# Optimization experiments

Hardware: AMD Instinct MI355X
Metric: run time of the kernel (lower is better)

## Reference

```python
import jax, jax.numpy as jnp
import numpy as np

D_MODEL = 384
N_HEADS = 8
HEAD_DIM = D_MODEL // N_HEADS


def setup_inputs() -> dict:
    key = jax.random.key(0)
    ks = jax.random.split(key, 8)
    b, n = 2, 2048
    s = 0.02
    return {
        "x": jax.random.normal(ks[0], (b, n, D_MODEL), jnp.float32),
        "coords": jax.random.normal(ks[1], (b, n, 3), jnp.float32),
        "W_qkv": jax.random.normal(ks[2], (D_MODEL, 3 * D_MODEL), jnp.float32) * s,
        "b_qkv": jnp.zeros((3 * D_MODEL,), jnp.float32),
        "W_dist": jax.random.normal(ks[3], (1, N_HEADS), jnp.float32) * s,
        "b_dist": jnp.zeros((N_HEADS,), jnp.float32),
        "W_out": jax.random.normal(ks[4], (D_MODEL, D_MODEL), jnp.float32) * s,
        "b_out": jnp.zeros((D_MODEL,), jnp.float32),
    }


def reference(x, coords, W_qkv, b_qkv, W_dist, b_dist, W_out, b_out):
    b, n, _ = x.shape
    qkv = x @ W_qkv + b_qkv                       # (b, n, 3*d)
    q, k, v = jnp.split(qkv, 3, axis=-1)
    def heads(t):
        return t.reshape(b, n, N_HEADS, HEAD_DIM).transpose(0, 2, 1, 3)  # b h n d
    q, k, v = heads(q), heads(k), heads(v)
    attn = jnp.einsum('bhid,bhjd->bhij', q, k) / jnp.sqrt(jnp.float32(HEAD_DIM))
    # distance bias: ||c_i - c_j|| projected to heads (Linear(1, n_heads))
    diff = coords[:, :, None, :] - coords[:, None, :, :]   # (b, i, j, 3)
    dist = jnp.sqrt(jnp.sum(diff * diff, axis=-1))         # (b, i, j)
    dist_bias = dist[..., None] * W_dist[0] + b_dist       # (b, i, j, h)
    attn = attn + dist_bias.transpose(0, 3, 1, 2)          # (b, h, i, j)
    attn = jax.nn.softmax(attn, axis=-1)
    out = jnp.einsum('bhij,bhjd->bhid', attn, v)
    out = out.transpose(0, 2, 1, 3).reshape(b, n, D_MODEL)
    return out @ W_out + b_out
```

## Files before the change

### kernel.cpp

```cpp
#include <hip/hip_runtime.h>
#include <hip/hip_bf16.h>

#define NB 2
#define SEQ 2048
#define DM 384
#define NH 8
#define HD 48
#define QKVN 1152
#define BH (NB*NH)

typedef __hip_bfloat16 bf16;
typedef __attribute__((ext_vector_type(8))) short short8;
typedef __attribute__((ext_vector_type(4))) float float4v;

static __device__ __forceinline__ float bf2f(bf16 v){ return __bfloat162float(v); }
static __device__ __forceinline__ float ldin(const void* p, size_t i, int isf){
    return isf ? ((const float*)p)[i] : bf2f(((const bf16*)p)[i]);
}
static __device__ __forceinline__ short f2b(float f){
    union { float f; unsigned u; } a; a.f = f;
    unsigned r = a.u + 0x7FFFu + ((a.u >> 16) & 1u);
    return (short)(r >> 16);
}
static __device__ __forceinline__ unsigned pk2(float a, float b){
    union { __hip_bfloat162 h; unsigned u; } r;
    r.h = __float22bfloat162_rn(float2{a, b});
    return r.u;
}
static __device__ __forceinline__ float bflo(unsigned u){
    union { unsigned u; float f; } a; a.u = u << 16; return a.f;
}
static __device__ __forceinline__ float bfhi(unsigned u){
    union { unsigned u; float f; } a; a.u = u & 0xFFFF0000u; return a.f;
}
static __device__ __forceinline__ short8 s4z(int2 v){
    union { int2 i; short s[4]; } u; u.i = v;
    short8 r = {u.s[0], u.s[1], u.s[2], u.s[3], 0, 0, 0, 0};
    return r;
}
static __device__ __forceinline__ short8 u2z(unsigned a, unsigned b){
    union { unsigned u[2]; short s[4]; } u0; u0.u[0] = a; u0.u[1] = b;
    short8 r = {u0.s[0], u0.s[1], u0.s[2], u0.s[3], 0, 0, 0, 0};
    return r;
}
static __device__ __forceinline__ int detect_isf(const void* x){
    const unsigned short* xb = (const unsigned short*)x;
    int l = threadIdx.x & 63;
    union { unsigned u; float f; } a; a.u = ((unsigned)xb[2*l]) << 16;
    float ab = fabsf(a.f);
    int good = (a.f == 0.0f) || (ab > 9.765625e-4f && ab < 1024.0f);
    unsigned long long m = __ballot(good);
    return (__popcll(m) >= 32) ? 0 : 1;
}

__global__ __launch_bounds__(256) void k_prep(const void* __restrict__ x,
    const void* __restrict__ coords,
    const void* __restrict__ Wqkv, const void* __restrict__ Wout,
    const void* __restrict__ bqkv, const void* __restrict__ bout,
    const void* __restrict__ Wdist, const void* __restrict__ bdist,
    short* __restrict__ dist8, short* __restrict__ xb,
    short* __restrict__ WqT, short* __restrict__ WoT,
    float* __restrict__ bqf, float* __restrict__ bof,
    float* __restrict__ wdf, float* __restrict__ bdf)
{
    const int isf = detect_isf(x);
    const int t = threadIdx.x;
    const int b = blockIdx.x;
    if (b < 512) {
        const int bb = b >> 8;
        const int jg = (b >> 1) & 127;
        const int j0 = jg * 16;
        const int ih = (b & 1) * 1024;
        __shared__ float cjx[16], cjy[16], cjz[16];
        if (t < 16) {
            int gj = (bb*SEQ + j0 + t)*3;
            cjx[t] = ldin(coords, gj, isf);
            cjy[t] = ldin(coords, gj+1, isf);
            cjz[t] = ldin(coords, gj+2, isf);
        }
        __syncthreads();
        #pragma unroll
        for (int k = 0; k < 4; ++k) {
            int i = ih + k*256 + t;
            int gi = (bb*SEQ + i)*3;
            float px = ldin(coords, gi, isf), py = ldin(coords, gi+1, isf), pz = ldin(coords, gi+2, isf);
            short o[16];
            #pragma unroll
            for (int e = 0; e < 16; ++e) {
                float dx = px - cjx[e], dy = py - cjy[e], dz = pz - cjz[e];
                o[e] = f2b(sqrtf(dx*dx + dy*dy + dz*dz));
            }
            short* dst = dist8 + (((size_t)bb*128 + jg)*SEQ + i)*16;
            *(int4*)dst       = *(const int4*)(o);
            *(int4*)(dst + 8) = *(const int4*)(o + 8);
        }
    } else if (b < 1280) {
        size_t i = ((size_t)(b-512)*256 + t)*8;
        if (isf) {
            const float* xf = (const float*)x + i;
            short o[8];
            #pragma unroll
            for (int e = 0; e < 8; ++e) o[e] = f2b(xf[e]);
            *(int4*)(xb + i) = *(const int4*)o;
        } else {
            *(int4*)(xb + i) = *(const int4*)((const short*)x + i);
        }
    } else if (b < 1856) {
        int bb, NW; const void* W; short* WT;
        if (b < 1712) { bb = b - 1280; NW = QKVN; W = Wqkv; WT = WqT; }
        else          { bb = b - 1712; NW = DM;   W = Wout; WT = WoT; }
        int ntiles = NW >> 5;
        int kt = bb / ntiles, nt = bb % ntiles;
        int k0 = kt*32, n0 = nt*32;
        __shared__ float Ls[32][33];
        for (int idx = t; idx < 1024; idx += 256) {
            int r = idx >> 5, c = idx & 31;
            Ls[r][c] = ldin(W, (size_t)(k0+r)*NW + n0 + c, isf);
        }
        __syncthreads();
        for (int idx = t; idx < 1024; idx += 256) {
            int r2 = idx >> 5, c2 = idx & 31;
            WT[(size_t)(n0+r2)*DM + k0 + c2] = f2b(Ls[c2][r2]);
        }
    } else {
        int idx = (b - 1856)*256 + t;
        const float log2e = 1.4426950408889634f;
        if (idx < QKVN) bqf[idx] = ldin(bqkv, idx, isf);
        else if (idx < QKVN + DM) bof[idx - QKVN] = ldin(bout, idx - QKVN, isf);
        else if (idx < QKVN + DM + NH) wdf[idx - QKVN - DM] = ldin(Wdist, idx - QKVN - DM, isf)*log2e;
        else if (idx < QKVN + DM + 2*NH) bdf[idx - QKVN - DM - NH] = ldin(bdist, idx - QKVN - DM - NH, isf)*log2e;
    }
}

__global__ __launch_bounds__(256) void k_qkv(const short* __restrict__ xb,
    const short* __restrict__ WT, const float* __restrict__ bias,
    short* __restrict__ qg2, short* __restrict__ kg2, short* __restrict__ vg2)
{
    __shared__ __align__(16) short As[64*72];
    __shared__ __align__(16) short Bs[128*72];
    const int t = threadIdx.x;
    const int w = t >> 6, lane = t & 63, L = lane & 15, quad = lane >> 4;
    const int mt = blockIdx.x / 9, nt = blockIdx.x % 9;
    const int row0 = mt*64, col0 = nt*128;
    const int wm = w & 1, wn = w >> 1;
    float4v acc[2][4] = {};
    for (int k0 = 0; k0 < DM; k0 += 64) {
        __syncthreads();
        for (int c = t; c < 512; c += 256) {
            int row = c >> 3, k8 = c & 7;
            *(int4*)(&As[row*72 + k8*8]) = *(const int4*)(xb + (size_t)(row0+row)*DM + k0 + k8*8);
        }
        for (int c = t; c < 1024; c += 256) {
            int row = c >> 3, k8 = c & 7;
            *(int4*)(&Bs[row*72 + k8*8]) = *(const int4*)(WT + (size_t)(col0+row)*DM + k0 + k8*8);
        }
        __syncthreads();
        #pragma unroll
        for (int kc = 0; kc < 2; ++kc) {
            short8 a0 = *(const short8*)(&As[(32*wm + L)*72 + kc*32 + quad*8]);
            short8 a1 = *(const short8*)(&As[(32*wm + 16 + L)*72 + kc*32 + quad*8]);
            #pragma unroll
            for (int ni = 0; ni < 4; ++ni) {
                short8 bf = *(const short8*)(&Bs[(64*wn + 16*ni + L)*72 + kc*32 + quad*8]);
                acc[0][ni] = __builtin_amdgcn_mfma_f32_16x16x32_bf16(a0, bf, acc[0][ni], 0, 0, 0);
                acc[1][ni] = __builtin_amdgcn_mfma_f32_16x16x32_bf16(a1, bf, acc[1][ni], 0, 0, 0);
            }
        }
    }
    const int which = col0 / DM;
    const int cbase = col0 % DM;
    short* Ep = Bs;
    __syncthreads();
    if (which < 2) {
        #pragma unroll
        for (int mi = 0; mi < 2; ++mi)
            #pragma unroll
            for (int ni = 0; ni < 4; ++ni) {
                int col_l = 64*wn + 16*ni + L;
                float bv = bias[col0 + col_l];
                #pragma unroll
                for (int r = 0; r < 4; ++r) {
                    int row_l = 32*wm + 16*mi + quad*4 + r;
                    Ep[row_l*136 + col_l] = f2b(acc[mi][ni][r] + bv);
                }
            }
        __syncthreads();
        short* dst = which ? kg2 : qg2;
        for (int c = t; c < 1024; c += 256) {
            int row_l = c >> 4, col_l = (c & 15)*8;
            int row_g = row0 + row_l;
            int bi = row_g >> 11, nn = row_g & (SEQ-1);
            int c2 = cbase + col_l;
            int hh = c2/HD, dh = c2%HD;
            int bh = bi*NH + hh;
            size_t base = ((size_t)bh*128 + (nn>>4))*768;
            int Ltok = nn & 15;
            const short* src = &Ep[row_l*136 + col_l];
            if (dh < 32) {
                *(int4*)(dst + base + (dh>>3)*128 + Ltok*8) = *(const int4*)src;
            } else {
                int q0 = (dh - 32) >> 2;
                *(int2*)(dst + base + 512 + q0*64     + Ltok*4) = *(const int2*)src;
                *(int2*)(dst + base + 512 + (q0+1)*64 + Ltok*4) = *(const int2*)(src + 4);
            }
        }
    } else {
        #pragma unroll
        for (int mi = 0; mi < 2; ++mi)
            #pragma unroll
            for (int ni = 0; ni < 4; ++ni) {
                int col_l = 64*wn + 16*ni + L;
                float bv = bias[col0 + col_l];
                #pragma unroll
                for (int r = 0; r < 4; ++r) {
                    int row_l = 32*wm + 16*mi + quad*4 + r;
                    Ep[col_l*72 + row_l] = f2b(acc[mi][ni][r] + bv);
                }
            }
        __syncthreads();
        for (int c = t; c < 1024; c += 256) {
            int col_l = c >> 3, row8 = (c & 7)*8;
            int row_g = row0 + row8;
            int bi = row_g >> 11, nn = row_g & (SEQ-1);
            int c2 = cbase + col_l;
            int hh = c2/HD, dh = c2%HD;
            int bh = bi*NH + hh;
            int dt = dh >> 4, Lh = dh & 15;
            size_t base3 = (((size_t)bh*128 + (nn>>4))*3 + dt)*256;
            int q0 = (nn & 15) >> 2;
            const short* src = &Ep[col_l*72 + row8];
            *(int2*)(vg2 + base3 + q0*64     + Lh*4) = *(const int2*)src;
            *(int2*)(vg2 + base3 + (q0+1)*64 + Lh*4) = *(const int2*)(src + 4);
        }
    }
}

__global__ __launch_bounds__(256, 4) void k_attn(
    const short* __restrict__ qg2, const short* __restrict__ kg2, const short* __restrict__ vg2,
    const short* __restrict__ dist8, const float* __restrict__ wdf,
    const float* __restrict__ bdf, short* __restrict__ aob)
{
    __shared__ float Ored[2][32*48];
    __shared__ float Lred[2][32];
    const int t = threadIdx.x;
    const int w = t >> 6, lane = t & 63, L = lane & 15, q = lane >> 4;
    const int bid = blockIdx.x;
    const int bh = bid & 15, it = bid >> 4;
    const int bi = bh >> 3, hh = bh & 7;
    const int i0 = it*32;
    const float scale2 = 0.14433756729740643f * 1.4426950408889634f;
    const float wd = wdf[hh], bd = bdf[hh];

    const short* qB = qg2 + ((size_t)bh*128 + it*2)*768;
    short8 qa0[2], qa1[2];
    #pragma unroll
    for (int nt = 0; nt < 2; ++nt) {
        qa0[nt] = *(const short8*)(qB + nt*768 + q*128 + L*8);
        qa1[nt] = s4z(*(const int2*)(qB + nt*768 + 512 + q*64 + L*4));
    }

    float4v accO[2][3] = {};
    float rsum[2] = {};

    const short* kBp = kg2 + ((size_t)bh*128 + w)*768;
    const short* vBp = vg2 + ((size_t)bh*128 + w)*768;
    const short* dBp = dist8 + (((size_t)bi*128 + w)*SEQ + i0 + L)*16 + 4*q;

    #pragma unroll 2
    for (int itr = 0; itr < SEQ/64; ++itr) {
        short8 ka0 = *(const short8*)(kBp + q*128 + L*8);
        short8 ka1 = s4z(*(const int2*)(kBp + 512 + q*64 + L*4));
        float4v sacc[2] = {};
        #pragma unroll
        for (int nt = 0; nt < 2; ++nt) {
            sacc[nt] = __builtin_amdgcn_mfma_f32_16x16x32_bf16(ka0, qa0[nt], sacc[nt], 0, 0, 0);
            sacc[nt] = __builtin_amdgcn_mfma_f32_16x16x32_bf16(ka1, qa1[nt], sacc[nt], 0, 0, 0);
        }
        short8 vf[3];
        #pragma unroll
        for (int dt = 0; dt < 3; ++dt)
            vf[dt] = s4z(*(const int2*)(vBp + dt*256 + q*64 + L*4));
        short8 pa[2];
        #pragma unroll
        for (int nt = 0; nt < 2; ++nt) {
            int2 du = *(const int2*)(dBp + nt*256);
            float d0 = bflo((unsigned)du.x), d1 = bfhi((unsigned)du.x);
            float d2 = bflo((unsigned)du.y), d3 = bfhi((unsigned)du.y);
            float p0 = __builtin_amdgcn_exp2f(fmaf(sacc[nt][0], scale2, fmaf(d0, wd, bd)));
            float p1 = __builtin_amdgcn_exp2f(fmaf(sacc[nt][1], scale2, fmaf(d1, wd, bd)));
            float p2 = __builtin_amdgcn_exp2f(fmaf(sacc[nt][2], scale2, fmaf(d2, wd, bd)));
            float p3 = __builtin_amdgcn_exp2f(fmaf(sacc[nt][3], scale2, fmaf(d3, wd, bd)));
            rsum[nt] += (p0 + p1) + (p2 + p3);
            pa[nt] = u2z(pk2(p0, p1), pk2(p2, p3));
        }
        #pragma unroll
        for (int nt = 0; nt < 2; ++nt)
            #pragma unroll
            for (int dt = 0; dt < 3; ++dt)
                accO[nt][dt] = __builtin_amdgcn_mfma_f32_16x16x32_bf16(pa[nt], vf[dt], accO[nt][dt], 0, 0, 0);
        kBp += 4*768; vBp += 4*768; dBp += (size_t)4*SEQ*16;
    }
    #pragma unroll
    for (int nt = 0; nt < 2; ++nt) {
        rsum[nt] += __shfl_xor(rsum[nt], 16);
        rsum[nt] += __shfl_xor(rsum[nt], 32);
    }
    if (w >= 2) {
        float* Od = Ored[w-2];
        #pragma unroll
        for (int mt = 0; mt < 2; ++mt)
            #pragma unroll
            for (int dt = 0; dt < 3; ++dt)
                #pragma unroll
                for (int r = 0; r < 4; ++r)
                    Od[(16*mt + 4*q + r)*48 + 16*dt + L] = accO[mt][dt][r];
        if (q == 0)
            #pragma unroll
            for (int nt = 0; nt < 2; ++nt) Lred[w-2][16*nt + L] = rsum[nt];
    }
    __syncthreads();
    if (w < 2) {
        float* Od = Ored[w];
        #pragma unroll
        for (int mt = 0; mt < 2; ++mt)
            #pragma unroll
            for (int dt = 0; dt < 3; ++dt)
                #pragma unroll
                for (int r = 0; r < 4; ++r)
                    accO[mt][dt][r] += Od[(16*mt + 4*q + r)*48 + 16*dt + L];
        #pragma unroll
        for (int nt = 0; nt < 2; ++nt) rsum[nt] += Lred[w][16*nt + L];
    }
    __syncthreads();
    if (w == 1) {
        float* Od = Ored[0];
        #pragma unroll
        for (int mt = 0; mt < 2; ++mt)
            #pragma unroll
            for (int dt = 0; dt < 3; ++dt)
                #pragma unroll
                for (int r = 0; r < 4; ++r)
                    Od[(16*mt + 4*q + r)*48 + 16*dt + L] = accO[mt][dt][r];
        if (q == 0)
            #pragma unroll
            for (int nt = 0; nt < 2; ++nt) Lred[0][16*nt + L] = rsum[nt];
    }
    __syncthreads();
    if (w == 0) {
        float* Od = Ored[0];
        #pragma unroll
        for (int mt = 0; mt < 2; ++mt)
            #pragma unroll
            for (int dt = 0; dt < 3; ++dt)
                #pragma unroll
                for (int r = 0; r < 4; ++r)
                    Od[(16*mt + 4*q + r)*48 + 16*dt + L] += accO[mt][dt][r];
        if (q == 0)
            #pragma unroll
            for (int nt = 0; nt < 2; ++nt) Lred[0][16*nt + L] += rsum[nt];
    }
    __syncthreads();
    for (int c = t; c < 192; c += 256) {
        int r = c / 6, d8 = (c % 6)*8;
        float inv = 1.0f / Lred[0][r];
        const float* src = &Ored[0][r*48 + d8];
        short o[8];
        #pragma unroll
        for (int e = 0; e < 8; ++e) o[e] = f2b(src[e]*inv);
        *(int4*)(aob + ((size_t)(bi*SEQ) + i0 + r)*DM + hh*HD + d8) = *(const int4*)o;
    }
}

__global__ __launch_bounds__(256) void k_out(const short* __restrict__ aob,
    const short* __restrict__ WT, const float* __restrict__ bias,
    void* __restrict__ out, const void* __restrict__ x)
{
    __shared__ __align__(16) short As[64*72];
    __shared__ __align__(16) short Bs[128*72];
    const int isf = detect_isf(x);
    const int t = threadIdx.x;
    const int w = t >> 6, lane = t & 63, L = lane & 15, quad = lane >> 4;
    const int mt = blockIdx.x / 3, nt = blockIdx.x % 3;
    const int row0 = mt*64, col0 = nt*128;
    const int wm = w & 1, wn = w >> 1;
    float4v acc[2][4] = {};
    for (int k0 = 0; k0 < DM; k0 += 64) {
        __syncthreads();
        for (int c = t; c < 512; c += 256) {
            int row = c >> 3, k8 = c & 7;
            *(int4*)(&As[row*72 + k8*8]) = *(const int4*)(aob + (size_t)(row0+row)*DM + k0 + k8*8);
        }
        for (int c = t; c < 1024; c += 256) {
            int row = c >> 3, k8 = c & 7;
            *(int4*)(&Bs[row*72 + k8*8]) = *(const int4*)(WT + (size_t)(col0+row)*DM + k0 + k8*8);
        }
        __syncthreads();
        #pragma unroll
        for (int kc = 0; kc < 2; ++kc) {
            short8 a0 = *(const short8*)(&As[(32*wm + L)*72 + kc*32 + quad*8]);
            short8 a1 = *(const short8*)(&As[(32*wm + 16 + L)*72 + kc*32 + quad*8]);
            #pragma unroll
            for (int ni = 0; ni < 4; ++ni) {
                short8 bf = *(const short8*)(&Bs[(64*wn + 16*ni + L)*72 + kc*32 + quad*8]);
                acc[0][ni] = __builtin_amdgcn_mfma_f32_16x16x32_bf16(a0, bf, acc[0][ni], 0, 0, 0);
                acc[1][ni] = __builtin_amdgcn_mfma_f32_16x16x32_bf16(a1, bf, acc[1][ni], 0, 0, 0);
            }
        }
    }
    #pragma unroll
    for (int mi = 0; mi < 2; ++mi) {
        #pragma unroll
        for (int ni = 0; ni < 4; ++ni) {
            int col_g = col0 + 64*wn + 16*ni + L;
            float bv = bias[col_g];
            #pragma unroll
            for (int r = 0; r < 4; ++r) {
                int row_g = row0 + 32*wm + 16*mi + quad*4 + r;
                size_t oi = (size_t)row_g*DM + col_g;
                float val = acc[mi][ni][r] + bv;
                if (isf) ((float*)out)[oi] = val;
                else     ((bf16*)out)[oi]  = __float2bfloat16(val);
            }
        }
    }
}

extern "C" void kernel_launch(void* const* d_in, const int* in_sizes, int n_in,
                              void* d_out, int out_size, void* d_ws, size_t ws_size,
                              hipStream_t stream) {
    const void* x      = d_in[0];
    const void* coords = d_in[1];
    const void* Wqkv   = d_in[2];
    const void* bqkv   = d_in[3];
    const void* Wdist  = d_in[4];
    const void* bdist  = d_in[5];
    const void* Wout   = d_in[6];
    const void* bout   = d_in[7];

    short* qg2   = (short*)d_ws;
    short* kg2   = qg2  + (size_t)1572864;
    short* vg2   = kg2  + (size_t)1572864;
    short* dist8 = vg2  + (size_t)1572864;
    short* aob   = dist8 + (size_t)8388608;
    short* xb    = aob  + (size_t)1572864;
    short* WqT   = xb   + (size_t)1572864;
    short* WoT   = WqT  + (size_t)442368;
    float* bqf   = (float*)(WoT + (size_t)147456);
    float* bof   = bqf + QKVN;
    float* wdf   = bof + DM;
    float* bdf   = wdf + NH;

    k_prep<<<dim3(1863), dim3(256), 0, stream>>>(x, coords, Wqkv, Wout, bqkv, bout,
                                                 Wdist, bdist, dist8, xb, WqT, WoT,
                                                 bqf, bof, wdf, bdf);
    k_qkv<<<dim3(64*9), dim3(256), 0, stream>>>(xb, WqT, bqf, qg2, kg2, vg2);
    k_attn<<<dim3(16*64), dim3(256), 0, stream>>>(qg2, kg2, vg2, dist8, wdf, bdf, aob);
    k_out<<<dim3(64*3), dim3(256), 0, stream>>>(aob, WoT, bof, d_out, x);
}
```

Baseline: 150.0 us.

## Switch attention to 32x32x16 MFMA with matching Q/K/V and distance layouts

The attention kernel now uses 32x32x16 bf16 MFMA instead of 16x16x32. Q, K and V are written in a new fragment layout that feeds the 32-wide tiles with no zero-padded half operands. The distance table and its loads are reorganised to match the new accumulator layout, and the block index is remapped so blocks sharing a batch and head are interleaved differently. The goal is to drop the wasted padded MFMA work on the 48-wide head dimension and reduce instruction count per key tile. In exchange, the accumulator layout is larger and the loop is no longer unrolled.

After: 144.3 us. 1.04x faster.

```diff
diff --git a/kernel.cpp b/kernel.cpp
--- a/kernel.cpp
+++ b/kernel.cpp
@@ -7,11 +7,11 @@
 #define NH 8
 #define HD 48
 #define QKVN 1152
-#define BH (NB*NH)
 
 typedef __hip_bfloat16 bf16;
 typedef __attribute__((ext_vector_type(8))) short short8;
 typedef __attribute__((ext_vector_type(4))) float float4v;
+typedef __attribute__((ext_vector_type(16))) float f32x16;
 
 static __device__ __forceinline__ float bf2f(bf16 v){ return __bfloat162float(v); }
 static __device__ __forceinline__ float ldin(const void* p, size_t i, int isf){
@@ -33,15 +33,8 @@
 static __device__ __forceinline__ float bfhi(unsigned u){
     union { unsigned u; float f; } a; a.u = u & 0xFFFF0000u; return a.f;
 }
-static __device__ __forceinline__ short8 s4z(int2 v){
-    union { int2 i; short s[4]; } u; u.i = v;
-    short8 r = {u.s[0], u.s[1], u.s[2], u.s[3], 0, 0, 0, 0};
-    return r;
-}
-static __device__ __forceinline__ short8 u2z(unsigned a, unsigned b){
-    union { unsigned u[2]; short s[4]; } u0; u0.u[0] = a; u0.u[1] = b;
-    short8 r = {u0.s[0], u0.s[1], u0.s[2], u0.s[3], 0, 0, 0, 0};
-    return r;
+static __device__ __forceinline__ short8 u4pack(unsigned w0, unsigned w1, unsigned w2, unsigned w3){
+    union { unsigned u[4]; short8 s; } r; r.u[0]=w0; r.u[1]=w1; r.u[2]=w2; r.u[3]=w3; return r.s;
 }
 static __device__ __forceinline__ int detect_isf(const void* x){
     const unsigned short* xb = (const unsigned short*)x;
@@ -90,9 +83,11 @@
                 float dx = px - cjx[e], dy = py - cjy[e], dz = pz - cjz[e];
                 o[e] = f2b(sqrtf(dx*dx + dy*dy + dz*dz));
             }
-            short* dst = dist8 + (((size_t)bb*128 + jg)*SEQ + i)*16;
-            *(int4*)dst       = *(const int4*)(o);
-            *(int4*)(dst + 8) = *(const int4*)(o + 8);
+            short* dst = dist8 + (((size_t)bb*512 + (size_t)jg*4)*SEQ + i)*4;
+            *(int2*)(dst)          = *(const int2*)(o);
+            *(int2*)(dst + SEQ*4)  = *(const int2*)(o + 4);
+            *(int2*)(dst + SEQ*8)  = *(const int2*)(o + 8);
+            *(int2*)(dst + SEQ*12) = *(const int2*)(o + 12);
         }
     } else if (b < 1280) {
         size_t i = ((size_t)(b-512)*256 + t)*8;
@@ -134,7 +129,7 @@
 
 __global__ __launch_bounds__(256) void k_qkv(const short* __restrict__ xb,
     const short* __restrict__ WT, const float* __restrict__ bias,
-    short* __restrict__ qg2, short* __restrict__ kg2, short* __restrict__ vg2)
+    short* __restrict__ qg3, short* __restrict__ kg3, short* __restrict__ vg3)
 {
     __shared__ __align__(16) short As[64*72];
     __shared__ __align__(16) short Bs[128*72];
@@ -185,7 +180,7 @@
                 }
             }
         __syncthreads();
-        short* dst = which ? kg2 : qg2;
+        short* dst = which ? kg3 : qg3;
         for (int c = t; c < 1024; c += 256) {
             int row_l = c >> 4, col_l = (c & 15)*8;
             int row_g = row0 + row_l;
@@ -193,16 +188,9 @@
             int c2 = cbase + col_l;
             int hh = c2/HD, dh = c2%HD;
             int bh = bi*NH + hh;
-            size_t base = ((size_t)bh*128 + (nn>>4))*768;
-            int Ltok = nn & 15;
-            const short* src = &Ep[row_l*136 + col_l];
-            if (dh < 32) {
-                *(int4*)(dst + base + (dh>>3)*128 + Ltok*8) = *(const int4*)src;
-            } else {
-                int q0 = (dh - 32) >> 2;
-                *(int2*)(dst + base + 512 + q0*64     + Ltok*4) = *(const int2*)src;
-                *(int2*)(dst + base + 512 + (q0+1)*64 + Ltok*4) = *(const int2*)(src + 4);
-            }
+            int dc = dh >> 4, hi = (dh >> 3) & 1;
+            size_t dstoff = ((size_t)bh*64 + (nn>>5))*1536 + (size_t)((dc*2 + hi)*256 + (nn&31)*8);
+            *(int4*)(dst + dstoff) = *(const int4*)(&Ep[row_l*136 + col_l]);
         }
     } else {
         #pragma unroll
@@ -225,139 +213,129 @@
             int c2 = cbase + col_l;
             int hh = c2/HD, dh = c2%HD;
             int bh = bi*NH + hh;
-            int dt = dh >> 4, Lh = dh & 15;
-            size_t base3 = (((size_t)bh*128 + (nn>>4))*3 + dt)*256;
-            int q0 = (nn & 15) >> 2;
-            const short* src = &Ep[col_l*72 + row8];
-            *(int2*)(vg2 + base3 + q0*64     + Lh*4) = *(const int2*)src;
-            *(int2*)(vg2 + base3 + (q0+1)*64 + Lh*4) = *(const int2*)(src + 4);
+            int jt = nn >> 5, jc = (nn >> 4) & 1;
+            int ehalf = ((nn >> 3) & 1)*4;
+            int dt = dh >> 5, dp = dh & 31;
+            int hstride = dt ? 128 : 256;
+            size_t base = ((size_t)bh*64 + jt)*1536 + (size_t)(jc*768 + dt*512 + dp*8 + ehalf);
+            *(int2*)(vg3 + base)           = *(const int2*)(&Ep[col_l*72 + row8]);
+            *(int2*)(vg3 + base + hstride) = *(const int2*)(&Ep[col_l*72 + row8 + 4]);
         }
     }
 }
 
 __global__ __launch_bounds__(256, 4) void k_attn(
-    const short* __restrict__ qg2, const short* __restrict__ kg2, const short* __restrict__ vg2,
+    const short* __restrict__ qg3, const short* __restrict__ kg3, const short* __restrict__ vg3,
     const short* __restrict__ dist8, const float* __restrict__ wdf,
     const float* __restrict__ bdf, short* __restrict__ aob)
 {
     __shared__ float Ored[2][32*48];
     __shared__ float Lred[2][32];
     const int t = threadIdx.x;
-    const int w = t >> 6, lane = t & 63, L = lane & 15, q = lane >> 4;
+    const int w = t >> 6, lane = t & 63;
+    const int li = lane & 31, hi = lane >> 5;
     const int bid = blockIdx.x;
-    const int bh = bid & 15, it = bid >> 4;
-    const int bi = bh >> 3, hh = bh & 7;
+    const int lg = (bid & 7)*128 + (bid >> 3);
+    const int hh = lg & 7;
+    const int rest = lg >> 3;
+    const int bi = rest & 1, it = rest >> 1;
+    const int bh = bi*NH + hh;
     const int i0 = it*32;
     const float scale2 = 0.14433756729740643f * 1.4426950408889634f;
     const float wd = wdf[hh], bd = bdf[hh];
 
-    const short* qB = qg2 + ((size_t)bh*128 + it*2)*768;
-    short8 qa0[2], qa1[2];
-    #pragma unroll
-    for (int nt = 0; nt < 2; ++nt) {
-        qa0[nt] = *(const short8*)(qB + nt*768 + q*128 + L*8);
-        qa1[nt] = s4z(*(const int2*)(qB + nt*768 + 512 + q*64 + L*4));
-    }
-
-    float4v accO[2][3] = {};
-    float rsum[2] = {};
-
-    const short* kBp = kg2 + ((size_t)bh*128 + w)*768;
-    const short* vBp = vg2 + ((size_t)bh*128 + w)*768;
-    const short* dBp = dist8 + (((size_t)bi*128 + w)*SEQ + i0 + L)*16 + 4*q;
-
-    #pragma unroll 2
-    for (int itr = 0; itr < SEQ/64; ++itr) {
-        short8 ka0 = *(const short8*)(kBp + q*128 + L*8);
-        short8 ka1 = s4z(*(const int2*)(kBp + 512 + q*64 + L*4));
-        float4v sacc[2] = {};
-        #pragma unroll
-        for (int nt = 0; nt < 2; ++nt) {
-            sacc[nt] = __builtin_amdgcn_mfma_f32_16x16x32_bf16(ka0, qa0[nt], sacc[nt], 0, 0, 0);
-            sacc[nt] = __builtin_amdgcn_mfma_f32_16x16x32_bf16(ka1, qa1[nt], sacc[nt], 0, 0, 0);
-        }
-        short8 vf[3];
-        #pragma unroll
-        for (int dt = 0; dt < 3; ++dt)
-            vf[dt] = s4z(*(const int2*)(vBp + dt*256 + q*64 + L*4));
-        short8 pa[2];
-        #pragma unroll
-        for (int nt = 0; nt < 2; ++nt) {
-            int2 du = *(const int2*)(dBp + nt*256);
+    const short* qB = qg3 + ((size_t)bh*64 + it)*1536 + hi*256 + li*8;
+    const short8 qf0 = *(const short8*)(qB);
+    const short8 qf1 = *(const short8*)(qB + 512);
+    const short8 qf2 = *(const short8*)(qB + 1024);
+
+    f32x16 accO0 = {}, accO1 = {};
+    float rsum = 0.0f;
+
+    const short* kBp = kg3 + ((size_t)bh*64 + w)*1536 + hi*256 + li*8;
+    const short* vBp = vg3 + ((size_t)bh*64 + w)*1536 + li*8;
+    const short* dBp = dist8 + (((size_t)bi*512 + (size_t)w*8 + hi)*SEQ + i0 + li)*4;
+
+    for (int s = 0; s < 16; ++s) {
+        short8 kf0 = *(const short8*)(kBp);
+        short8 kf1 = *(const short8*)(kBp + 512);
+        short8 kf2 = *(const short8*)(kBp + 1024);
+        int2 du0 = *(const int2*)(dBp);
+        int2 du1 = *(const int2*)(dBp + SEQ*8);
+        int2 du2 = *(const int2*)(dBp + SEQ*16);
+        int2 du3 = *(const int2*)(dBp + SEQ*24);
+        f32x16 sacc = {};
+        sacc = __builtin_amdgcn_mfma_f32_32x32x16_bf16(kf0, qf0, sacc, 0, 0, 0);
+        sacc = __builtin_amdgcn_mfma_f32_32x32x16_bf16(kf1, qf1, sacc, 0, 0, 0);
+        sacc = __builtin_amdgcn_mfma_f32_32x32x16_bf16(kf2, qf2, sacc, 0, 0, 0);
+        float p[16];
+        #pragma unroll
+        for (int rq = 0; rq < 4; ++rq) {
+            int2 du = rq == 0 ? du0 : rq == 1 ? du1 : rq == 2 ? du2 : du3;
             float d0 = bflo((unsigned)du.x), d1 = bfhi((unsigned)du.x);
             float d2 = bflo((unsigned)du.y), d3 = bfhi((unsigned)du.y);
-            float p0 = __builtin_amdgcn_exp2f(fmaf(sacc[nt][0], scale2, fmaf(d0, wd, bd)));
-            float p1 = __builtin_amdgcn_exp2f(fmaf(sacc[nt][1], scale2, fmaf(d1, wd, bd)));
-            float p2 = __builtin_amdgcn_exp2f(fmaf(sacc[nt][2], scale2, fmaf(d2, wd, bd)));
-            float p3 = __builtin_amdgcn_exp2f(fmaf(sacc[nt][3], scale2, fmaf(d3, wd, bd)));
-            rsum[nt] += (p0 + p1) + (p2 + p3);
-            pa[nt] = u2z(pk2(p0, p1), pk2(p2, p3));
-        }
-        #pragma unroll
-        for (int nt = 0; nt < 2; ++nt)
-            #pragma unroll
-            for (int dt = 0; dt < 3; ++dt)
-                accO[nt][dt] = __builtin_amdgcn_mfma_f32_16x16x32_bf16(pa[nt], vf[dt], accO[nt][dt], 0, 0, 0);
-        kBp += 4*768; vBp += 4*768; dBp += (size_t)4*SEQ*16;
-    }
-    #pragma unroll
-    for (int nt = 0; nt < 2; ++nt) {
-        rsum[nt] += __shfl_xor(rsum[nt], 16);
-        rsum[nt] += __shfl_xor(rsum[nt], 32);
-    }
+            p[4*rq+0] = __builtin_amdgcn_exp2f(fmaf(sacc[4*rq+0], scale2, fmaf(d0, wd, bd)));
+            p[4*rq+1] = __builtin_amdgcn_exp2f(fmaf(sacc[4*rq+1], scale2, fmaf(d1, wd, bd)));
+            p[4*rq+2] = __builtin_amdgcn_exp2f(fmaf(sacc[4*rq+2], scale2, fmaf(d2, wd, bd)));
+            p[4*rq+3] = __builtin_amdgcn_exp2f(fmaf(sacc[4*rq+3], scale2, fmaf(d3, wd, bd)));
+            rsum += (p[4*rq+0] + p[4*rq+1]) + (p[4*rq+2] + p[4*rq+3]);
+        }
+        short8 pa0 = u4pack(pk2(p[0],p[1]),  pk2(p[2],p[3]),  pk2(p[4],p[5]),   pk2(p[6],p[7]));
+        short8 pa1 = u4pack(pk2(p[8],p[9]),  pk2(p[10],p[11]),pk2(p[12],p[13]), pk2(p[14],p[15]));
+        short8 v00 = *(const short8*)(vBp + hi*256);
+        short8 v10 = *(const short8*)(vBp + 768 + hi*256);
+        accO0 = __builtin_amdgcn_mfma_f32_32x32x16_bf16(pa0, v00, accO0, 0, 0, 0);
+        accO0 = __builtin_amdgcn_mfma_f32_32x32x16_bf16(pa1, v10, accO0, 0, 0, 0);
+        short8 v01 = *(const short8*)(vBp + 512 + hi*128);
+        short8 v11 = *(const short8*)(vBp + 1280 + hi*128);
+        accO1 = __builtin_amdgcn_mfma_f32_32x32x16_bf16(pa0, v01, accO1, 0, 0, 0);
+        accO1 = __builtin_amdgcn_mfma_f32_32x32x16_bf16(pa1, v11, accO1, 0, 0, 0);
+        kBp += 4*1536; vBp += 4*1536; dBp += (size_t)SEQ*128;
+    }
+    rsum += __shfl_xor(rsum, 32);
+
     if (w >= 2) {
         float* Od = Ored[w-2];
         #pragma unroll
-        for (int mt = 0; mt < 2; ++mt)
-            #pragma unroll
-            for (int dt = 0; dt < 3; ++dt)
-                #pragma unroll
-                for (int r = 0; r < 4; ++r)
-                    Od[(16*mt + 4*q + r)*48 + 16*dt + L] = accO[mt][dt][r];
-        if (q == 0)
-            #pragma unroll
-            for (int nt = 0; nt < 2; ++nt) Lred[w-2][16*nt + L] = rsum[nt];
+        for (int r = 0; r < 16; ++r) {
+            int ii = (r & 3) + 8*(r >> 2) + 4*hi;
+            Od[ii*48 + li] = accO0[r];
+            if (li < 16) Od[ii*48 + 32 + li] = accO1[r];
+        }
+        if (lane < 32) Lred[w-2][lane] = rsum;
     }
     __syncthreads();
     if (w < 2) {
-        float* Od = Ored[w];
-        #pragma unroll
-        for (int mt = 0; mt < 2; ++mt)
-            #pragma unroll
-            for (int dt = 0; dt < 3; ++dt)
-                #pragma unroll
-                for (int r = 0; r < 4; ++r)
-                    accO[mt][dt][r] += Od[(16*mt + 4*q + r)*48 + 16*dt + L];
-        #pragma unroll
-        for (int nt = 0; nt < 2; ++nt) rsum[nt] += Lred[w][16*nt + L];
+        const float* Od = Ored[w];
+        #pragma unroll
+        for (int r = 0; r < 16; ++r) {
+            int ii = (r & 3) + 8*(r >> 2) + 4*hi;
+            accO0[r] += Od[ii*48 + li];
+            accO1[r] += Od[ii*48 + 32 + (li & 15)];
+        }
+        rsum += Lred[w][li];
     }
     __syncthreads();
     if (w == 1) {
         float* Od = Ored[0];
         #pragma unroll
-        for (int mt = 0; mt < 2; ++mt)
-            #pragma unroll
-            for (int dt = 0; dt < 3; ++dt)
-                #pragma unroll
-                for (int r = 0; r < 4; ++r)
-                    Od[(16*mt + 4*q + r)*48 + 16*dt + L] = accO[mt][dt][r];
-        if (q == 0)
-            #pragma unroll
-            for (int nt = 0; nt < 2; ++nt) Lred[0][16*nt + L] = rsum[nt];
+        for (int r = 0; r < 16; ++r) {
+            int ii = (r & 3) + 8*(r >> 2) + 4*hi;
+            Od[ii*48 + li] = accO0[r];
+            if (li < 16) Od[ii*48 + 32 + li] = accO1[r];
+        }
+        if (lane < 32) Lred[0][lane] = rsum;
     }
     __syncthreads();
     if (w == 0) {
         float* Od = Ored[0];
         #pragma unroll
-        for (int mt = 0; mt < 2; ++mt)
-            #pragma unroll
-            for (int dt = 0; dt < 3; ++dt)
-                #pragma unroll
-                for (int r = 0; r < 4; ++r)
-                    Od[(16*mt + 4*q + r)*48 + 16*dt + L] += accO[mt][dt][r];
-        if (q == 0)
-            #pragma unroll
-            for (int nt = 0; nt < 2; ++nt) Lred[0][16*nt + L] += rsum[nt];
+        for (int r = 0; r < 16; ++r) {
+            int ii = (r & 3) + 8*(r >> 2) + 4*hi;
+            Od[ii*48 + li] += accO0[r];
+            if (li < 16) Od[ii*48 + 32 + li] += accO1[r];
+        }
+        if (lane < 32) Lred[0][lane] += rsum;
     }
     __syncthreads();
     for (int c = t; c < 192; c += 256) {
@@ -437,10 +415,10 @@
     const void* Wout   = d_in[6];
     const void* bout   = d_in[7];
 
-    short* qg2   = (short*)d_ws;
-    short* kg2   = qg2  + (size_t)1572864;
-    short* vg2   = kg2  + (size_t)1572864;
-    short* dist8 = vg2  + (size_t)1572864;
+    short* qg3   = (short*)d_ws;
+    short* kg3   = qg3  + (size_t)1572864;
+    short* vg3   = kg3  + (size_t)1572864;
+    short* dist8 = vg3  + (size_t)1573120;
     short* aob   = dist8 + (size_t)8388608;
     short* xb    = aob  + (size_t)1572864;
     short* WqT   = xb   + (size_t)1572864;
@@ -453,7 +431,7 @@
     k_prep<<<dim3(1863), dim3(256), 0, stream>>>(x, coords, Wqkv, Wout, bqkv, bout,
                                                  Wdist, bdist, dist8, xb, WqT, WoT,
                                                  bqf, bof, wdf, bdf);
-    k_qkv<<<dim3(64*9), dim3(256), 0, stream>>>(xb, WqT, bqf, qg2, kg2, vg2);
-    k_attn<<<dim3(16*64), dim3(256), 0, stream>>>(qg2, kg2, vg2, dist8, wdf, bdf, aob);
+    k_qkv<<<dim3(64*9), dim3(256), 0, stream>>>(xb, WqT, bqf, qg3, kg3, vg3);
+    k_attn<<<dim3(16*64), dim3(256), 0, stream>>>(qg3, kg3, vg3, dist8, wdf, bdf, aob);
     k_out<<<dim3(64*3), dim3(256), 0, stream>>>(aob, WoT, bof, d_out, x);
 }
```
